# Optimization experiments

Measured on AMD Instinct MI355X. Metric: run time of the kernel, lower is better.

Reference implementation:

```python
import jax, jax.numpy as jnp
import numpy as np

N_ACTIONS = 4
HIDDEN = 32

def setup_inputs() -> dict:
    key = jax.random.key(0)
    ks = jax.random.split(key, 8)
    B, T = 2048, 1024
    prev_actions_onehot = jax.random.uniform(ks[0], (B, T, N_ACTIONS), dtype=jnp.float32)
    prev_rewards = jax.random.normal(ks[1], (B, T, 1), dtype=jnp.float32)
    in_dim = N_ACTIONS + 1
    s_ih = 1.0 / np.sqrt(HIDDEN)
    W_ih = jax.random.uniform(ks[2], (HIDDEN, in_dim), jnp.float32, -s_ih, s_ih)
    W_hh = jax.random.uniform(ks[3], (HIDDEN, HIDDEN), jnp.float32, -s_ih, s_ih)
    b_ih = jax.random.uniform(ks[4], (HIDDEN,), jnp.float32, -s_ih, s_ih)
    b_hh = jax.random.uniform(ks[5], (HIDDEN,), jnp.float32, -s_ih, s_ih)
    W_ro = jax.random.uniform(ks[6], (N_ACTIONS, HIDDEN), jnp.float32, -s_ih, s_ih)
    b_ro = jax.random.uniform(ks[7], (N_ACTIONS,), jnp.float32, -s_ih, s_ih)
    return {
        'prev_actions_onehot': prev_actions_onehot,
        'prev_rewards': prev_rewards,
        'W_ih': W_ih, 'W_hh': W_hh, 'b_ih': b_ih, 'b_hh': b_hh,
        'W_ro': W_ro, 'b_ro': b_ro,
    }

def reference(prev_actions_onehot, prev_rewards, W_ih, W_hh, b_ih, b_hh, W_ro, b_ro):
    # x_seq: [B, T, n_actions+1]
    x_seq = jnp.concatenate([prev_actions_onehot, prev_rewards], axis=-1)
    B = x_seq.shape[0]
    # Precompute the input projection for all steps (parallel): [B, T, H]
    x_proj = jnp.einsum('bti,hi->bth', x_seq, W_ih) + b_ih + b_hh
    h0 = jnp.zeros((B, HIDDEN), dtype=x_seq.dtype)

    def step(h, xp_t):
        # xp_t: [B, H] (already contains x@W_ih^T + b_ih + b_hh)
        h_new = jnp.tanh(xp_t + h @ W_hh.T)
        return h_new, h_new

    # scan over time: move T to leading axis
    h_T, hs = jax.lax.scan(step, h0, jnp.swapaxes(x_proj, 0, 1))
    hs = jnp.swapaxes(hs, 0, 1)  # [B, T, H]
    logits_seq = jnp.einsum('bth,ah->bta', hs, W_ro) + b_ro  # [B, T, n_actions]
    return logits_seq, h_T
```

## Files before the change

### kernel.cpp

```cpp
#include <hip/hip_runtime.h>

#define H 32
#define GPB 8
#define PITCH 48

__device__ __forceinline__ float fast_tanh(float x) {
    float e = __builtin_amdgcn_exp2f(x * 2.8853900817779268f);
    float r = __builtin_amdgcn_rcpf(e + 1.0f);
    return fmaf(-2.0f, r, 1.0f);
}

#define QFMA(acc, p, w, q) \
    asm("v_fmac_f32_dpp %0, %1, %2 quad_perm:[" #q "," #q "," #q "," #q "] row_mask:0xf bank_mask:0xf" \
        : "+v"(acc) : "v"(p), "v"(w))

#define CH8(acc, q) \
    QFMA(acc, pN[0], whh[8*q+0], q); QFMA(acc, pN[1], whh[8*q+1], q); \
    QFMA(acc, pN[2], whh[8*q+2], q); QFMA(acc, pN[3], whh[8*q+3], q); \
    QFMA(acc, pN[4], whh[8*q+4], q); QFMA(acc, pN[5], whh[8*q+5], q); \
    QFMA(acc, pN[6], whh[8*q+6], q); QFMA(acc, pN[7], whh[8*q+7], q)

#define DPPMOV(x, ctrl) \
    __int_as_float(__builtin_amdgcn_update_dpp(0, __float_as_int(x), (ctrl), 0xf, 0xf, true))
#define ROW_SHR1 0x111
#define ROW_SHR2 0x112
#define ROW_SHR4 0x114

__global__ __launch_bounds__(256, 1) void rnn_fused(
    const float* __restrict__ onehot,
    const float* __restrict__ rewards,
    const float* __restrict__ W_ih,
    const float* __restrict__ W_hh,
    const float* __restrict__ b_ih,
    const float* __restrict__ b_hh,
    const float* __restrict__ W_ro,
    const float* __restrict__ b_ro,
    float* __restrict__ out_logits,
    float* __restrict__ out_hT,
    int T)
{
    const int tid = threadIdx.x;
    const int j   = tid & 31;
    const int g   = tid >> 5;
    const int b   = blockIdx.x * GPB + g;
    const int qp  = j & 3;
    const int r   = j >> 3;
    const bool hi = ((j >> 2) & 1) != 0;
    const bool writer = (j & 7) == 7;

    __shared__ __align__(16) float hx[GPB * PITCH];
    float* lds_wr = &hx[g * PITCH + j];
    const float4* lds_rd0 = (const float4*)&hx[g * PITCH + qp * 8];
    const float4* lds_rd1 = lds_rd0 + 1;

    float whh[H];
#pragma unroll
    for (int k = 0; k < 8; ++k) {
        float4 w = *(const float4*)(W_hh + j * H + 4 * k);
        whh[4*k+0] = w.x; whh[4*k+1] = w.y; whh[4*k+2] = w.z; whh[4*k+3] = w.w;
    }
    const float wih0 = W_ih[j*5+0], wih1 = W_ih[j*5+1], wih2 = W_ih[j*5+2],
                wih3 = W_ih[j*5+3], wih4 = W_ih[j*5+4];
    const float bias = b_ih[j] + b_hh[j];
    const float4 wr4 = *(const float4*)(W_ro + r * H + qp * 8 + (hi ? 4 : 0));
    const float bro = b_ro[r];

    const float* oh_ptr = onehot  + (size_t)b * T * 4;
    const float* rw_ptr = rewards + (size_t)b * T;
    float*       lg_ptr = out_logits + (size_t)b * T * 4;

    float4 oh0 = *(const float4*)(oh_ptr + 0);
    float4 oh1 = *(const float4*)(oh_ptr + 4);
    float4 oh2 = *(const float4*)(oh_ptr + 8);
    float4 oh3 = *(const float4*)(oh_ptr + 12);
    float4 rw  = *(const float4*)(rw_ptr);

    float hj = 0.0f;
    float pA[8], pB[8];

    auto readout = [&](const float (&p)[8], int t) {
        float s0 = hi ? p[4] : p[0];
        float s1 = hi ? p[5] : p[1];
        float s2 = hi ? p[6] : p[2];
        float s3 = hi ? p[7] : p[3];
        float s = fmaf(s3, wr4.w, fmaf(s2, wr4.z, fmaf(s1, wr4.y, s0 * wr4.x)));
        s += DPPMOV(s, ROW_SHR1);
        s += DPPMOV(s, ROW_SHR2);
        s += DPPMOV(s, ROW_SHR4);
        if (writer) lg_ptr[(size_t)t * 4 + r] = s + bro;
    };

    auto step = [&](float (&pN)[8], const float (&pO)[8], float xp, int t, bool ro) {
        *lds_wr = hj;
        float4 v0 = *lds_rd0;
        float4 v1 = *lds_rd1;
        pN[0]=v0.x; pN[1]=v0.y; pN[2]=v0.z; pN[3]=v0.w;
        pN[4]=v1.x; pN[5]=v1.y; pN[6]=v1.z; pN[7]=v1.w;
        if (ro) readout(pO, t - 2);
        float a0 = xp, a1 = 0.f, a2 = 0.f, a3 = 0.f;
        CH8(a0, 0);
        CH8(a1, 1);
        CH8(a2, 2);
        CH8(a3, 3);
        hj = fast_tanh((a0 + a1) + (a2 + a3));
    };

    {
        float xp0 = fmaf(oh0.x,wih0, fmaf(oh0.y,wih1, fmaf(oh0.z,wih2, fmaf(oh0.w,wih3, fmaf(rw.x,wih4, bias)))));
        float xp1 = fmaf(oh1.x,wih0, fmaf(oh1.y,wih1, fmaf(oh1.z,wih2, fmaf(oh1.w,wih3, fmaf(rw.y,wih4, bias)))));
        float xp2 = fmaf(oh2.x,wih0, fmaf(oh2.y,wih1, fmaf(oh2.z,wih2, fmaf(oh2.w,wih3, fmaf(rw.z,wih4, bias)))));
        float xp3 = fmaf(oh3.x,wih0, fmaf(oh3.y,wih1, fmaf(oh3.z,wih2, fmaf(oh3.w,wih3, fmaf(rw.w,wih4, bias)))));
        oh0 = *(const float4*)(oh_ptr + 16);
        oh1 = *(const float4*)(oh_ptr + 20);
        oh2 = *(const float4*)(oh_ptr + 24);
        oh3 = *(const float4*)(oh_ptr + 28);
        rw  = *(const float4*)(rw_ptr + 4);
        step(pA, pB, xp0, 0, false);
        step(pB, pA, xp1, 1, false);
        step(pA, pB, xp2, 2, true);
        step(pB, pA, xp3, 3, true);
    }

    for (int tb = 4; tb < T; tb += 4) {
        float xp0 = fmaf(oh0.x,wih0, fmaf(oh0.y,wih1, fmaf(oh0.z,wih2, fmaf(oh0.w,wih3, fmaf(rw.x,wih4, bias)))));
        float xp1 = fmaf(oh1.x,wih0, fmaf(oh1.y,wih1, fmaf(oh1.z,wih2, fmaf(oh1.w,wih3, fmaf(rw.y,wih4, bias)))));
        float xp2 = fmaf(oh2.x,wih0, fmaf(oh2.y,wih1, fmaf(oh2.z,wih2, fmaf(oh2.w,wih3, fmaf(rw.z,wih4, bias)))));
        float xp3 = fmaf(oh3.x,wih0, fmaf(oh3.y,wih1, fmaf(oh3.z,wih2, fmaf(oh3.w,wih3, fmaf(rw.w,wih4, bias)))));
        if (tb + 4 < T) {
            oh0 = *(const float4*)(oh_ptr + (size_t)(tb + 4) * 4);
            oh1 = *(const float4*)(oh_ptr + (size_t)(tb + 5) * 4);
            oh2 = *(const float4*)(oh_ptr + (size_t)(tb + 6) * 4);
            oh3 = *(const float4*)(oh_ptr + (size_t)(tb + 7) * 4);
            rw  = *(const float4*)(rw_ptr + tb + 4);
        }
        step(pA, pB, xp0, tb + 0, true);
        step(pB, pA, xp1, tb + 1, true);
        step(pA, pB, xp2, tb + 2, true);
        step(pB, pA, xp3, tb + 3, true);
    }

    readout(pB, T - 2);
    *lds_wr = hj;
    {
        float4 v0 = *lds_rd0;
        float4 v1 = *lds_rd1;
        pA[0]=v0.x; pA[1]=v0.y; pA[2]=v0.z; pA[3]=v0.w;
        pA[4]=v1.x; pA[5]=v1.y; pA[6]=v1.z; pA[7]=v1.w;
    }
    readout(pA, T - 1);
    out_hT[(size_t)b * H + j] = hj;

}

extern "C" void kernel_launch(void* const* d_in, const int* in_sizes, int n_in,
                              void* d_out, int out_size, void* d_ws, size_t ws_size,
                              hipStream_t stream) {
    const float* onehot  = (const float*)d_in[0];
    const float* rewards = (const float*)d_in[1];
    const float* W_ih    = (const float*)d_in[2];
    const float* W_hh    = (const float*)d_in[3];
    const float* b_ih    = (const float*)d_in[4];
    const float* b_hh    = (const float*)d_in[5];
    const float* W_ro    = (const float*)d_in[6];
    const float* b_ro    = (const float*)d_in[7];

    const int T = 1024;
    const int B = in_sizes[1] / T;

    float* out_logits = (float*)d_out;
    float* out_hT     = (float*)d_out + (size_t)B * T * 4;

    dim3 block(256);
    dim3 grid(B / GPB);
    rnn_fused<<<grid, block, 0, stream>>>(onehot, rewards, W_ih, W_hh,
                                          b_ih, b_hh, W_ro, b_ro,
                                          out_logits, out_hT, T);
}
```

Baseline: 322.2 us.

## Interleave two independent batch recurrences per 32-lane group to hide latency

Each 32-lane half-wave now carries two batch rows and interleaves their recurrence steps, so one row's LDS publish and tanh latency can overlap with the other row's FMA chain. Blocks shrink to a single 64-thread wave handling 4 batches, which gives 512 blocks instead of 256. The readout now uses the freshly read hidden state rather than a two-step delayed buffer. The cost is doubled register pressure for prefetched inputs, and the dependence chains still rely on implicit wave-level ordering of LDS accesses.

```diff
diff --git a/kernel.cpp b/kernel.cpp
--- a/kernel.cpp
+++ b/kernel.cpp
@@ -1,8 +1,7 @@
 #include <hip/hip_runtime.h>
 
 #define H 32
-#define GPB 8
-#define PITCH 48
+#define PITCH 40
 
 __device__ __forceinline__ float fast_tanh(float x) {
     float e = __builtin_amdgcn_exp2f(x * 2.8853900817779268f);
@@ -26,7 +25,7 @@
 #define ROW_SHR2 0x112
 #define ROW_SHR4 0x114
 
-__global__ __launch_bounds__(256, 1) void rnn_fused(
+__global__ __launch_bounds__(64, 1) void rnn_fused(
     const float* __restrict__ onehot,
     const float* __restrict__ rewards,
     const float* __restrict__ W_ih,
@@ -40,45 +39,52 @@
     int T)
 {
     const int tid = threadIdx.x;
-    const int j   = tid & 31;
-    const int g   = tid >> 5;
-    const int b   = blockIdx.x * GPB + g;
-    const int qp  = j & 3;
-    const int r   = j >> 3;
-    const bool hi = ((j >> 2) & 1) != 0;
-    const bool writer = (j & 7) == 7;
+    const int u  = tid & 31;
+    const int g  = tid >> 5;
+    const int qp = u & 3;
+    const int r  = u >> 3;
+    const bool hi = ((u >> 2) & 1) != 0;
+    const bool writer = (u & 7) == 7;
 
-    __shared__ __align__(16) float hx[GPB * PITCH];
-    float* lds_wr = &hx[g * PITCH + j];
-    const float4* lds_rd0 = (const float4*)&hx[g * PITCH + qp * 8];
-    const float4* lds_rd1 = lds_rd0 + 1;
+    const int b0 = blockIdx.x * 4 + g * 2;
+    const int b1 = b0 + 1;
+
+    __shared__ __align__(16) float hx[4 * PITCH];
+    float* wr0 = &hx[(2 * g + 0) * PITCH + u];
+    float* wr1 = &hx[(2 * g + 1) * PITCH + u];
+    const float4* rd0 = (const float4*)&hx[(2 * g + 0) * PITCH + qp * 8];
+    const float4* rd1 = (const float4*)&hx[(2 * g + 1) * PITCH + qp * 8];
 
     float whh[H];
 #pragma unroll
     for (int k = 0; k < 8; ++k) {
-        float4 w = *(const float4*)(W_hh + j * H + 4 * k);
+        float4 w = *(const float4*)(W_hh + u * H + 4 * k);
         whh[4*k+0] = w.x; whh[4*k+1] = w.y; whh[4*k+2] = w.z; whh[4*k+3] = w.w;
     }
-    const float wih0 = W_ih[j*5+0], wih1 = W_ih[j*5+1], wih2 = W_ih[j*5+2],
-                wih3 = W_ih[j*5+3], wih4 = W_ih[j*5+4];
-    const float bias = b_ih[j] + b_hh[j];
+    const float wih0 = W_ih[u*5+0], wih1 = W_ih[u*5+1], wih2 = W_ih[u*5+2],
+                wih3 = W_ih[u*5+3], wih4 = W_ih[u*5+4];
+    const float bias = b_ih[u] + b_hh[u];
     const float4 wr4 = *(const float4*)(W_ro + r * H + qp * 8 + (hi ? 4 : 0));
     const float bro = b_ro[r];
 
-    const float* oh_ptr = onehot  + (size_t)b * T * 4;
-    const float* rw_ptr = rewards + (size_t)b * T;
-    float*       lg_ptr = out_logits + (size_t)b * T * 4;
+    const float* ohp0 = onehot  + (size_t)b0 * T * 4;
+    const float* ohp1 = onehot  + (size_t)b1 * T * 4;
+    const float* rwp0 = rewards + (size_t)b0 * T;
+    const float* rwp1 = rewards + (size_t)b1 * T;
+    float*       lgp0 = out_logits + (size_t)b0 * T * 4;
+    float*       lgp1 = out_logits + (size_t)b1 * T * 4;
 
-    float4 oh0 = *(const float4*)(oh_ptr + 0);
-    float4 oh1 = *(const float4*)(oh_ptr + 4);
-    float4 oh2 = *(const float4*)(oh_ptr + 8);
-    float4 oh3 = *(const float4*)(oh_ptr + 12);
-    float4 rw  = *(const float4*)(rw_ptr);
+    float4 A0 = *(const float4*)(ohp0 + 0), A1 = *(const float4*)(ohp0 + 4);
+    float4 A2 = *(const float4*)(ohp0 + 8), A3 = *(const float4*)(ohp0 + 12);
+    float4 Ar = *(const float4*)(rwp0);
+    float4 B0 = *(const float4*)(ohp1 + 0), B1 = *(const float4*)(ohp1 + 4);
+    float4 B2 = *(const float4*)(ohp1 + 8), B3 = *(const float4*)(ohp1 + 12);
+    float4 Br = *(const float4*)(rwp1);
 
-    float hj = 0.0f;
-    float pA[8], pB[8];
+    float h0 = 0.0f, h1 = 0.0f;
+    float4 v00, v01, v10, v11;
 
-    auto readout = [&](const float (&p)[8], int t) {
+    auto readout_store = [&](const float (&p)[8], float* lgp, int t) {
         float s0 = hi ? p[4] : p[0];
         float s1 = hi ? p[5] : p[1];
         float s2 = hi ? p[6] : p[2];
@@ -87,69 +93,80 @@
         s += DPPMOV(s, ROW_SHR1);
         s += DPPMOV(s, ROW_SHR2);
         s += DPPMOV(s, ROW_SHR4);
-        if (writer) lg_ptr[(size_t)t * 4 + r] = s + bro;
+        if (writer) lgp[(size_t)t * 4 + r] = s + bro;
     };
 
-    auto step = [&](float (&pN)[8], const float (&pO)[8], float xp, int t, bool ro) {
-        *lds_wr = hj;
-        float4 v0 = *lds_rd0;
-        float4 v1 = *lds_rd1;
-        pN[0]=v0.x; pN[1]=v0.y; pN[2]=v0.z; pN[3]=v0.w;
-        pN[4]=v1.x; pN[5]=v1.y; pN[6]=v1.z; pN[7]=v1.w;
-        if (ro) readout(pO, t - 2);
+    auto compute = [&](float4 v0, float4 v1, float xp, float* lgp, int tm1,
+                       bool ro) -> float {
+        float pN[8] = {v0.x, v0.y, v0.z, v0.w, v1.x, v1.y, v1.z, v1.w};
+        if (ro) readout_store(pN, lgp, tm1);
         float a0 = xp, a1 = 0.f, a2 = 0.f, a3 = 0.f;
         CH8(a0, 0);
         CH8(a1, 1);
         CH8(a2, 2);
         CH8(a3, 3);
-        hj = fast_tanh((a0 + a1) + (a2 + a3));
+        return fast_tanh((a0 + a1) + (a2 + a3));
     };
 
+#define PUBLISH0(h) { *wr0 = (h); v00 = rd0[0]; v01 = rd0[1]; }
+#define PUBLISH1(h) { *wr1 = (h); v10 = rd1[0]; v11 = rd1[1]; }
+
+#define STEP(xpA, xpB, tm1, ro) { \
+    h0 = compute(v00, v01, (xpA), lgp0, (tm1), (ro)); PUBLISH0(h0); \
+    h1 = compute(v10, v11, (xpB), lgp1, (tm1), (ro)); PUBLISH1(h1); }
+
+#define XP(oh, rwc) fmaf((oh).x, wih0, fmaf((oh).y, wih1, fmaf((oh).z, wih2, \
+                     fmaf((oh).w, wih3, fmaf((rwc), wih4, bias)))))
+
+    PUBLISH0(0.0f);
+    PUBLISH1(0.0f);
+
     {
-        float xp0 = fmaf(oh0.x,wih0, fmaf(oh0.y,wih1, fmaf(oh0.z,wih2, fmaf(oh0.w,wih3, fmaf(rw.x,wih4, bias)))));
-        float xp1 = fmaf(oh1.x,wih0, fmaf(oh1.y,wih1, fmaf(oh1.z,wih2, fmaf(oh1.w,wih3, fmaf(rw.y,wih4, bias)))));
-        float xp2 = fmaf(oh2.x,wih0, fmaf(oh2.y,wih1, fmaf(oh2.z,wih2, fmaf(oh2.w,wih3, fmaf(rw.z,wih4, bias)))));
-        float xp3 = fmaf(oh3.x,wih0, fmaf(oh3.y,wih1, fmaf(oh3.z,wih2, fmaf(oh3.w,wih3, fmaf(rw.w,wih4, bias)))));
-        oh0 = *(const float4*)(oh_ptr + 16);
-        oh1 = *(const float4*)(oh_ptr + 20);
-        oh2 = *(const float4*)(oh_ptr + 24);
-        oh3 = *(const float4*)(oh_ptr + 28);
-        rw  = *(const float4*)(rw_ptr + 4);
-        step(pA, pB, xp0, 0, false);
-        step(pB, pA, xp1, 1, false);
-        step(pA, pB, xp2, 2, true);
-        step(pB, pA, xp3, 3, true);
+        float xA0 = XP(A0, Ar.x), xA1 = XP(A1, Ar.y), xA2 = XP(A2, Ar.z), xA3 = XP(A3, Ar.w);
+        float xB0 = XP(B0, Br.x), xB1 = XP(B1, Br.y), xB2 = XP(B2, Br.z), xB3 = XP(B3, Br.w);
+        A0 = *(const float4*)(ohp0 + 16); A1 = *(const float4*)(ohp0 + 20);
+        A2 = *(const float4*)(ohp0 + 24); A3 = *(const float4*)(ohp0 + 28);
+        Ar = *(const float4*)(rwp0 + 4);
+        B0 = *(const float4*)(ohp1 + 16); B1 = *(const float4*)(ohp1 + 20);
+        B2 = *(const float4*)(ohp1 + 24); B3 = *(const float4*)(ohp1 + 28);
+        Br = *(const float4*)(rwp1 + 4);
+        STEP(xA0, xB0, -1, false);
+        STEP(xA1, xB1,  0, true);
+        STEP(xA2, xB2,  1, true);
+        STEP(xA3, xB3,  2, true);
     }
 
     for (int tb = 4; tb < T; tb += 4) {
-        float xp0 = fmaf(oh0.x,wih0, fmaf(oh0.y,wih1, fmaf(oh0.z,wih2, fmaf(oh0.w,wih3, fmaf(rw.x,wih4, bias)))));
-        float xp1 = fmaf(oh1.x,wih0, fmaf(oh1.y,wih1, fmaf(oh1.z,wih2, fmaf(oh1.w,wih3, fmaf(rw.y,wih4, bias)))));
-        float xp2 = fmaf(oh2.x,wih0, fmaf(oh2.y,wih1, fmaf(oh2.z,wih2, fmaf(oh2.w,wih3, fmaf(rw.z,wih4, bias)))));
-        float xp3 = fmaf(oh3.x,wih0, fmaf(oh3.y,wih1, fmaf(oh3.z,wih2, fmaf(oh3.w,wih3, fmaf(rw.w,wih4, bias)))));
+        float xA0 = XP(A0, Ar.x), xA1 = XP(A1, Ar.y), xA2 = XP(A2, Ar.z), xA3 = XP(A3, Ar.w);
+        float xB0 = XP(B0, Br.x), xB1 = XP(B1, Br.y), xB2 = XP(B2, Br.z), xB3 = XP(B3, Br.w);
         if (tb + 4 < T) {
-            oh0 = *(const float4*)(oh_ptr + (size_t)(tb + 4) * 4);
-            oh1 = *(const float4*)(oh_ptr + (size_t)(tb + 5) * 4);
-            oh2 = *(const float4*)(oh_ptr + (size_t)(tb + 6) * 4);
-            oh3 = *(const float4*)(oh_ptr + (size_t)(tb + 7) * 4);
-            rw  = *(const float4*)(rw_ptr + tb + 4);
+            A0 = *(const float4*)(ohp0 + (size_t)(tb + 4) * 4);
+            A1 = *(const float4*)(ohp0 + (size_t)(tb + 5) * 4);
+            A2 = *(const float4*)(ohp0 + (size_t)(tb + 6) * 4);
+            A3 = *(const float4*)(ohp0 + (size_t)(tb + 7) * 4);
+            Ar = *(const float4*)(rwp0 + tb + 4);
+            B0 = *(const float4*)(ohp1 + (size_t)(tb + 4) * 4);
+            B1 = *(const float4*)(ohp1 + (size_t)(tb + 5) * 4);
+            B2 = *(const float4*)(ohp1 + (size_t)(tb + 6) * 4);
+            B3 = *(const float4*)(ohp1 + (size_t)(tb + 7) * 4);
+            Br = *(const float4*)(rwp1 + tb + 4);
         }
-        step(pA, pB, xp0, tb + 0, true);
-        step(pB, pA, xp1, tb + 1, true);
-        step(pA, pB, xp2, tb + 2, true);
-        step(pB, pA, xp3, tb + 3, true);
+        STEP(xA0, xB0, tb - 1, true);
+        STEP(xA1, xB1, tb + 0, true);
+        STEP(xA2, xB2, tb + 1, true);
+        STEP(xA3, xB3, tb + 2, true);
     }
 
-    readout(pB, T - 2);
-    *lds_wr = hj;
     {
-        float4 v0 = *lds_rd0;
-        float4 v1 = *lds_rd1;
-        pA[0]=v0.x; pA[1]=v0.y; pA[2]=v0.z; pA[3]=v0.w;
-        pA[4]=v1.x; pA[5]=v1.y; pA[6]=v1.z; pA[7]=v1.w;
+        float pN[8] = {v00.x, v00.y, v00.z, v00.w, v01.x, v01.y, v01.z, v01.w};
+        readout_store(pN, lgp0, T - 1);
     }
-    readout(pA, T - 1);
-    out_hT[(size_t)b * H + j] = hj;
-
+    {
+        float pN[8] = {v10.x, v10.y, v10.z, v10.w, v11.x, v11.y, v11.z, v11.w};
+        readout_store(pN, lgp1, T - 1);
+    }
+    out_hT[(size_t)b0 * H + u] = h0;
+    out_hT[(size_t)b1 * H + u] = h1;
 }
 
 extern "C" void kernel_launch(void* const* d_in, const int* in_sizes, int n_in,
@@ -170,8 +187,8 @@
     float* out_logits = (float*)d_out;
     float* out_hT     = (float*)d_out + (size_t)B * T * 4;
 
-    dim3 block(256);
-    dim3 grid(B / GPB);
+    dim3 block(64);
+    dim3 grid(B / 4);
     rnn_fused<<<grid, block, 0, stream>>>(onehot, rewards, W_ih, W_hh,
                                           b_ih, b_hh, W_ro, b_ro,
                                           out_logits, out_hT, T);
```

Result: slower. 468.5 us (+45.4%).
